# Performance work log

Measured on AMD Instinct MI355X. Metric: run time of the kernel, lower is better.

## Reference

```python
import jax, jax.numpy as jnp
import numpy as np

BATCH, SEQ, D_IN = 4, 2048, 1024
STATE, D_OUT, KX = 1024, 1024, 10


def setup_inputs() -> dict:
    key = jax.random.key(0)
    k0, k1, k2, k3, k4, k5 = jax.random.split(key, 6)
    inputs = jax.random.normal(k0, (BATCH, SEQ, D_IN), jnp.float32)
    h0 = jax.random.normal(k1, (STATE,), jnp.float32)
    A = jax.random.normal(k2, (STATE,), jnp.float32)
    A = A / jnp.max(jnp.abs(A))  # matches init_A / max|init_A|
    B = jax.random.normal(k3, (D_IN, STATE), jnp.float32) / D_IN
    C = jax.random.normal(k4, (STATE, D_OUT), jnp.float32) / STATE
    M = jax.random.normal(k5, (D_IN, D_OUT, KX), jnp.float32) / D_OUT
    return {"inputs": inputs, "h0": h0, "A": A, "B": B, "C": C, "M": M}


def compute_ar_x_preds(w, x):
    # w: (d_out, d_in, k); x: (b, l, d_in)
    d_out, d_in, k = w.shape
    b, l, _ = x.shape
    o = jnp.einsum('oik,bli->bklo', w, x)  # (b, k, l, d_out)
    shifts = jnp.arange(k)
    # roll slice i forward by i along the length axis
    o = jax.vmap(lambda oi, s: jnp.roll(oi, s, axis=1), in_axes=(1, 0), out_axes=1)(o, shifts)
    # triu mask: keep position t in slice i only if t >= i (causal AR)
    m = (jnp.arange(l)[None, :] >= shifts[:, None]).astype(o.dtype)  # (k, l)
    return jnp.sum(o * m[None, :, :, None], axis=1)  # (b, l, d_out)


def reference(inputs, h0, A, B, C, M):
    bsz = inputs.shape[0]
    h_init = jnp.broadcast_to(h0, (bsz, h0.shape[0]))  # h0.expand(bsz, state_dim)
    u_seq = jnp.swapaxes(inputs, 0, 1)  # (l, b, d_in)

    def step(h, u):
        h_new = A * h + u @ B  # diagonal recurrence
        return h_new, h_new

    _, hs = jax.lax.scan(step, h_init, u_seq)  # (l, b, state)
    all_h_t = jnp.swapaxes(hs, 0, 1)  # (b, l, state)
    lds_out = all_h_t @ C  # (b, l, d_out)
    ar = compute_ar_x_preds(M, inputs)
    return lds_out + ar
```

## Files before the change

kernel.cpp:

```cpp
#include <hip/hip_runtime.h>
#include <stdint.h>

typedef unsigned short u16;
typedef __attribute__((ext_vector_type(4))) float f32x4;
typedef __attribute__((ext_vector_type(8))) short s16x8;

#define BATCH 4
#define SEQ   2048
#define DIM   1024
#define KX    10
#define PAD   16
#define SEQP  (SEQ+PAD)

__device__ __forceinline__ u16 f2b(float f) {
    union { float f; uint32_t u; } v; v.f = f;
    uint32_t u = v.u + 0x7fffu + ((v.u >> 16) & 1u);
    return (u16)(u >> 16);
}
__device__ __forceinline__ float b2f(u16 h) {
    union { uint32_t u; float f; } v; v.u = ((uint32_t)h) << 16;
    return v.f;
}

__device__ __forceinline__ void llds16(const u16* g, u16* l) {
    __builtin_amdgcn_global_load_lds(
        (const __attribute__((address_space(1))) uint32_t*)g,
        (__attribute__((address_space(3))) uint32_t*)l, 16, 0, 0);
}

#define PREP_X_END  8256
#define PREP_C_END  10304
#define PREP_M_END  14400

__global__ __launch_bounds__(256) void k_prep(
    const float* __restrict__ x, const float* __restrict__ B,
    const float* __restrict__ C, const float* __restrict__ M,
    u16* __restrict__ Xpad, u16* __restrict__ Btr, u16* __restrict__ Wall)
{
    __shared__ float tile[32][33];
    const int bid = blockIdx.x, tid = threadIdx.x;

    if (bid < PREP_X_END) {
        int idx = bid * 256 + tid;
        long e = (long)idx * 4;
        int i = (int)(e & 1023);
        int row = (int)(e >> 10);
        int t = row % SEQP;
        int b = row / SEQP;
        ushort4 o;
        if (t < PAD) {
            o.x = 0; o.y = 0; o.z = 0; o.w = 0;
        } else {
            const float4 v = *(const float4*)(x + (((long)(b * SEQ + (t - PAD)) << 10) + i));
            o.x = f2b(v.x); o.y = f2b(v.y); o.z = f2b(v.z); o.w = f2b(v.w);
        }
        *(ushort4*)(Xpad + ((long)row << 10) + i) = o;
    } else if (bid < PREP_C_END) {
        const int tb = bid - PREP_X_END;
        const float* in = (tb < 1024) ? B : C;
        u16* out = (tb < 1024) ? Btr : Wall;
        int lb = tb & 1023;
        int bx = lb & 31, by = lb >> 5;
        int tx = tid & 31, ty = tid >> 5;
#pragma unroll
        for (int j = 0; j < 4; j++)
            tile[ty + j * 8][tx] = in[(long)(by * 32 + ty + j * 8) * 1024 + bx * 32 + tx];
        __syncthreads();
#pragma unroll
        for (int j = 0; j < 4; j++)
            out[(long)(bx * 32 + ty + j * 8) * 1024 + by * 32 + tx] = f2b(tile[tx][ty + j * 8]);
    } else {
        int idx = (bid - PREP_C_END) * 256 + tid;
        int o = idx >> 10, i = idx & 1023;
        const float* src = M + (long)idx * KX;
#pragma unroll
        for (int k = 0; k < KX; k++)
            Wall[((long)(k + 1) << 20) + ((long)o << 10) + i] = f2b(src[k]);
    }
}


__global__ void k_scan1(const u16* __restrict__ U, const float* __restrict__ A,
                        float* __restrict__ F) {
    int s = blockIdx.x * 256 + threadIdx.x;
    int bc = blockIdx.y;
    int b = bc >> 4, c = bc & 15;
    float a = A[s];
    const u16* u = U + (((long)(b * SEQ + c * 128)) << 10) + s;
    float f = 0.f;
#pragma unroll 8
    for (int j = 0; j < 128; j++) f = fmaf(a, f, b2f(u[(long)j << 10]));
    F[((long)bc << 10) + s] = f;
}

__global__ void k_scan2(const float* __restrict__ F, const float* __restrict__ A,
                        const float* __restrict__ h0, float* __restrict__ Carry) {
    int idx = blockIdx.x * 256 + threadIdx.x;
    int b = idx >> 10, s = idx & 1023;
    float a = A[s];
    float a128 = a;
#pragma unroll
    for (int q = 0; q < 7; q++) a128 *= a128;
    float carry = h0[s];
#pragma unroll
    for (int c = 0; c < 16; c++) {
        long off = ((long)(b * 16 + c) << 10) + s;
        Carry[off] = carry;
        carry = fmaf(a128, carry, F[off]);
    }
}

__global__ void k_scan3(u16* __restrict__ U, const float* __restrict__ A,
                        const float* __restrict__ Carry) {
    int s = blockIdx.x * 256 + threadIdx.x;
    int bc = blockIdx.y;
    int b = bc >> 4, c = bc & 15;
    float a = A[s];
    long base = (((long)(b * SEQ + c * 128)) << 10) + s;
    float h = Carry[((long)bc << 10) + s];
#pragma unroll 8
    for (int j = 0; j < 128; j++) {
        h = fmaf(a, h, b2f(U[base + ((long)j << 10)]));
        U[base + ((long)j << 10)] = f2b(h);
    }
}

__global__ __launch_bounds__(256, 4) void k_gemm(
    void* __restrict__ outv, const u16* __restrict__ Xpad,
    const u16* __restrict__ Hbf, const u16* __restrict__ W,
    int ngroups, int use_h, int bf16_out)
{
    __shared__ u16 smem[18432];

    const int tid  = threadIdx.x;
    const int wave = tid >> 6, lane = tid & 63;
    const int pair = wave >> 1, wm = wave & 1;
    const int quad = lane >> 4, l15 = lane & 15;

    const int col0 = blockIdx.x * 64;
    const int row0 = blockIdx.y * 128;
    const int bb = row0 >> 11;
    const long Xrow0 = (long)bb * SEQP + PAD + (row0 & (SEQ - 1));
    const long XslabBase = (Xrow0 - 16) << 10;
    const int lastg = ngroups - 1;

    f32x4 acc[4][4];
#pragma unroll
    for (int i = 0; i < 4; i++)
#pragma unroll
        for (int j = 0; j < 4; j++)
            acc[i][j] = (f32x4){0.f, 0.f, 0.f, 0.f};

    auto stageX2 = [&](int k0) {
#pragma unroll
        for (int p = 0; p < 2; p++) {
            const int kb = k0 + p * 512;
            u16* slab = smem + p * 5120;
#pragma unroll
            for (int q = 0; q < 2; q++) {
                int u = q * 256 + tid;
                int row = u >> 2;
                int kc = (u & 3) ^ (row & 3);
                llds16(Xpad + XslabBase + ((long)row << 10) + kb + kc * 8,
                       &slab[(q * 256 + wave * 64) * 8]);
            }
            {
                int u = 512 + tid;
                int row = u >> 2;
                int kc = (u & 3) ^ (row & 3);
                if (tid < 128)
                    llds16(Xpad + XslabBase + ((long)row << 10) + kb + kc * 8,
                           &slab[(512 + wave * 64) * 8]);
            }
        }
    };
    auto stageW2 = [&](int k0, int wsel, int parity) {
        const u16* Wg = W + ((long)wsel << 20) + ((long)col0 << 10);
#pragma unroll
        for (int p = 0; p < 2; p++) {
            int row = tid >> 2;
            int kc = (tid & 3) ^ (row & 3);
            llds16(Wg + ((long)row << 10) + (k0 + p * 512) + kc * 8,
                   &smem[10240 + (p * 2 + parity) * 2048 + wave * 64 * 8]);
        }
    };
    auto stageH2 = [&](int k0) {
        const u16* Hb = Hbf + ((long)row0 << 10);
#pragma unroll
        for (int p = 0; p < 2; p++) {
            const int kb = k0 + p * 512;
            u16* slab = smem + p * 5120;
#pragma unroll
            for (int q = 0; q < 2; q++) {
                int u = q * 256 + tid;
                int row = u >> 2;
                int kc = (u & 3) ^ (row & 3);
                llds16(Hb + ((long)row << 10) + kb + kc * 8,
                       &slab[(q * 256 + wave * 64) * 8]);
            }
        }
    };

    const u16* slab  = smem + pair * 5120;
    const u16* Wpair = smem + 10240 + pair * 2 * 2048;

    for (int k0 = 0; k0 < 512; k0 += 32) {
        stageX2(k0);
        stageW2(k0, use_h ? 1 : 0, 0);
        __syncthreads();

        for (int g = 0; g < ngroups; g++) {
            const bool isH = use_h && (g == lastg);
            if (isH) {
                stageH2(k0);
                __syncthreads();
            }
            if (g < lastg) {
                int gn = g + 1;
                int wsel = use_h ? ((gn == lastg) ? 0 : gn + 1) : gn;
                stageW2(k0, wsel, gn & 1);
            }

            const int rbase = isH ? 0 : (16 - g);
            const u16* Wrd = Wpair + (g & 1) * 2048;

            s16x8 af[4], bfr[4];
#pragma unroll
            for (int mi = 0; mi < 4; mi++) {
                int arow = rbase + wm * 64 + mi * 16 + l15;
                int kca = (quad ^ (arow & 3)) << 3;
                af[mi] = *(const s16x8*)&slab[arow * 32 + kca];
            }
#pragma unroll
            for (int ni = 0; ni < 4; ni++) {
                int brow = ni * 16 + l15;
                int kcb = (quad ^ (brow & 3)) << 3;
                bfr[ni] = *(const s16x8*)&Wrd[brow * 32 + kcb];
            }
#pragma unroll
            for (int mi = 0; mi < 4; mi++)
#pragma unroll
                for (int ni = 0; ni < 4; ni++)
                    acc[mi][ni] = __builtin_amdgcn_mfma_f32_16x16x32_bf16(
                        af[mi], bfr[ni], acc[mi][ni], 0, 0, 0);
            __syncthreads();
        }
    }

    float* scr = (float*)smem;
    if (pair == 1) {
#pragma unroll
        for (int mi = 0; mi < 4; mi++) {
            int rl = wm * 64 + mi * 16 + quad * 4;
#pragma unroll
            for (int ni = 0; ni < 4; ni++) {
                int c = ni * 16 + l15;
                f32x4 v = acc[mi][ni];
#pragma unroll
                for (int reg = 0; reg < 4; reg++)
                    scr[(rl + reg) * 64 + c] = v[reg];
            }
        }
    }
    __syncthreads();
    if (pair == 0) {
#pragma unroll
        for (int mi = 0; mi < 4; mi++) {
            int rl = wm * 64 + mi * 16 + quad * 4;
            int r = row0 + rl;
#pragma unroll
            for (int ni = 0; ni < 4; ni++) {
                int cl = ni * 16 + l15;
                int c = col0 + cl;
                f32x4 v = acc[mi][ni];
                if (bf16_out) {
                    u16* ob = (u16*)outv;
#pragma unroll
                    for (int reg = 0; reg < 4; reg++)
                        ob[((long)(r + reg) << 10) + c] =
                            f2b(v[reg] + scr[(rl + reg) * 64 + cl]);
                } else {
                    float* of = (float*)outv;
#pragma unroll
                    for (int reg = 0; reg < 4; reg++)
                        of[((long)(r + reg) << 10) + c] =
                            v[reg] + scr[(rl + reg) * 64 + cl];
                }
            }
        }
    }
}


extern "C" void kernel_launch(void* const* d_in, const int* in_sizes, int n_in,
                              void* d_out, int out_size, void* d_ws, size_t ws_size,
                              hipStream_t stream) {
    const float* x  = (const float*)d_in[0];
    const float* h0 = (const float*)d_in[1];
    const float* A  = (const float*)d_in[2];
    const float* B  = (const float*)d_in[3];
    const float* C  = (const float*)d_in[4];
    const float* M  = (const float*)d_in[5];
    float* out = (float*)d_out;

    char* ws = (char*)d_ws;
    u16*   Xpad  = (u16*)  (ws);
    u16*   Wall  = (u16*)  (ws + 16908288);
    u16*   Btr   = (u16*)  (ws + 39976960);
    u16*   Ubf   = (u16*)  (ws + 42074112);
    float* F     = (float*)(ws + 58851328);
    float* Carry = (float*)(ws + 59113472);

    k_prep<<<dim3(PREP_M_END), dim3(256), 0, stream>>>(x, B, C, M, Xpad, Btr, Wall);

    k_gemm<<<dim3(16, 64), dim3(256), 0, stream>>>(Ubf, Xpad, Ubf, Btr, 1, 0, 1);

    k_scan1<<<dim3(4, 64), dim3(256), 0, stream>>>(Ubf, A, F);
    k_scan2<<<dim3(16), dim3(256), 0, stream>>>(F, A, h0, Carry);
    k_scan3<<<dim3(4, 64), dim3(256), 0, stream>>>(Ubf, A, Carry);

    k_gemm<<<dim3(16, 64), dim3(256), 0, stream>>>(out, Xpad, Ubf, Wall, 11, 1, 0);
}
```

Measured before the change: 357.1 us.

## Vectorize scan kernels with 8-wide bf16 loads and change LDS swizzle pattern

The chunked scan kernels now process 8 state channels per thread with 16-byte vector loads and stores, using 64-step chunks (32 chunks per batch) instead of 128-step chunks, and scan2 is adjusted to a^64 accordingly. The GEMM's LDS XOR swizzle now uses (row>>1)&3 to cut bank conflicts on the 16-byte fragment reads. F and Carry are moved to reuse the Btr workspace region, which is dead after the first GEMM. The scan kernels launch only 128 blocks of 128 threads, which may underfill the GPU, and the workspace aliasing depends on Btr not being read later.

New measurement: 354.6 us. No clear change (-0.7%).

```diff
diff --git a/kernel.cpp b/kernel.cpp
--- a/kernel.cpp
+++ b/kernel.cpp
@@ -82,15 +82,23 @@
 
 __global__ void k_scan1(const u16* __restrict__ U, const float* __restrict__ A,
                         float* __restrict__ F) {
-    int s = blockIdx.x * 256 + threadIdx.x;
-    int bc = blockIdx.y;
-    int b = bc >> 4, c = bc & 15;
-    float a = A[s];
-    const u16* u = U + (((long)(b * SEQ + c * 128)) << 10) + s;
-    float f = 0.f;
-#pragma unroll 8
-    for (int j = 0; j < 128; j++) f = fmaf(a, f, b2f(u[(long)j << 10]));
-    F[((long)bc << 10) + s] = f;
+    const int sg = threadIdx.x;
+    const int bc = blockIdx.x;
+    const int b = bc >> 5, c = bc & 31;
+    const int s0 = sg << 3;
+    const float4 a0 = *(const float4*)(A + s0);
+    const float4 a1 = *(const float4*)(A + s0 + 4);
+    float a[8] = {a0.x, a0.y, a0.z, a0.w, a1.x, a1.y, a1.z, a1.w};
+    float f[8] = {0.f, 0.f, 0.f, 0.f, 0.f, 0.f, 0.f, 0.f};
+    const u16* u = U + (((long)(b * SEQ + c * 64)) << 10) + s0;
+#pragma unroll 4
+    for (int j = 0; j < 64; j++) {
+        s16x8 v = *(const s16x8*)(u + ((long)j << 10));
+#pragma unroll
+        for (int i = 0; i < 8; i++) f[i] = fmaf(a[i], f[i], b2f((u16)v[i]));
+    }
+    *(float4*)(F + ((long)bc << 10) + s0)     = (float4){f[0], f[1], f[2], f[3]};
+    *(float4*)(F + ((long)bc << 10) + s0 + 4) = (float4){f[4], f[5], f[6], f[7]};
 }
 
 __global__ void k_scan2(const float* __restrict__ F, const float* __restrict__ A,
@@ -98,30 +106,41 @@
     int idx = blockIdx.x * 256 + threadIdx.x;
     int b = idx >> 10, s = idx & 1023;
     float a = A[s];
-    float a128 = a;
-#pragma unroll
-    for (int q = 0; q < 7; q++) a128 *= a128;
+    float a64 = a;
+#pragma unroll
+    for (int q = 0; q < 6; q++) a64 *= a64;
     float carry = h0[s];
 #pragma unroll
-    for (int c = 0; c < 16; c++) {
-        long off = ((long)(b * 16 + c) << 10) + s;
+    for (int c = 0; c < 32; c++) {
+        long off = ((long)(b * 32 + c) << 10) + s;
         Carry[off] = carry;
-        carry = fmaf(a128, carry, F[off]);
+        carry = fmaf(a64, carry, F[off]);
     }
 }
 
 __global__ void k_scan3(u16* __restrict__ U, const float* __restrict__ A,
                         const float* __restrict__ Carry) {
-    int s = blockIdx.x * 256 + threadIdx.x;
-    int bc = blockIdx.y;
-    int b = bc >> 4, c = bc & 15;
-    float a = A[s];
-    long base = (((long)(b * SEQ + c * 128)) << 10) + s;
-    float h = Carry[((long)bc << 10) + s];
-#pragma unroll 8
-    for (int j = 0; j < 128; j++) {
-        h = fmaf(a, h, b2f(U[base + ((long)j << 10)]));
-        U[base + ((long)j << 10)] = f2b(h);
+    const int sg = threadIdx.x;
+    const int bc = blockIdx.x;
+    const int b = bc >> 5, c = bc & 31;
+    const int s0 = sg << 3;
+    const float4 a0 = *(const float4*)(A + s0);
+    const float4 a1 = *(const float4*)(A + s0 + 4);
+    float a[8] = {a0.x, a0.y, a0.z, a0.w, a1.x, a1.y, a1.z, a1.w};
+    float h[8];
+#pragma unroll
+    for (int i = 0; i < 8; i++) h[i] = Carry[((long)bc << 10) + s0 + i];
+    u16* u = U + (((long)(b * SEQ + c * 64)) << 10) + s0;
+#pragma unroll 4
+    for (int j = 0; j < 64; j++) {
+        s16x8 v = *(const s16x8*)(u + ((long)j << 10));
+        s16x8 w;
+#pragma unroll
+        for (int i = 0; i < 8; i++) {
+            h[i] = fmaf(a[i], h[i], b2f((u16)v[i]));
+            w[i] = (short)f2b(h[i]);
+        }
+        *(s16x8*)(u + ((long)j << 10)) = w;
     }
 }
 
@@ -160,14 +179,14 @@
             for (int q = 0; q < 2; q++) {
                 int u = q * 256 + tid;
                 int row = u >> 2;
-                int kc = (u & 3) ^ (row & 3);
+                int kc = (u & 3) ^ ((row >> 1) & 3);
                 llds16(Xpad + XslabBase + ((long)row << 10) + kb + kc * 8,
                        &slab[(q * 256 + wave * 64) * 8]);
             }
             {
                 int u = 512 + tid;
                 int row = u >> 2;
-                int kc = (u & 3) ^ (row & 3);
+                int kc = (u & 3) ^ ((row >> 1) & 3);
                 if (tid < 128)
                     llds16(Xpad + XslabBase + ((long)row << 10) + kb + kc * 8,
                            &slab[(512 + wave * 64) * 8]);
@@ -179,7 +198,7 @@
 #pragma unroll
         for (int p = 0; p < 2; p++) {
             int row = tid >> 2;
-            int kc = (tid & 3) ^ (row & 3);
+            int kc = (tid & 3) ^ ((row >> 1) & 3);
             llds16(Wg + ((long)row << 10) + (k0 + p * 512) + kc * 8,
                    &smem[10240 + (p * 2 + parity) * 2048 + wave * 64 * 8]);
         }
@@ -194,7 +213,7 @@
             for (int q = 0; q < 2; q++) {
                 int u = q * 256 + tid;
                 int row = u >> 2;
-                int kc = (u & 3) ^ (row & 3);
+                int kc = (u & 3) ^ ((row >> 1) & 3);
                 llds16(Hb + ((long)row << 10) + kb + kc * 8,
                        &slab[(q * 256 + wave * 64) * 8]);
             }
@@ -228,13 +247,13 @@
 #pragma unroll
             for (int mi = 0; mi < 4; mi++) {
                 int arow = rbase + wm * 64 + mi * 16 + l15;
-                int kca = (quad ^ (arow & 3)) << 3;
+                int kca = (quad ^ ((arow >> 1) & 3)) << 3;
                 af[mi] = *(const s16x8*)&slab[arow * 32 + kca];
             }
 #pragma unroll
             for (int ni = 0; ni < 4; ni++) {
                 int brow = ni * 16 + l15;
-                int kcb = (quad ^ (brow & 3)) << 3;
+                int kcb = (quad ^ ((brow >> 1) & 3)) << 3;
                 bfr[ni] = *(const s16x8*)&Wrd[brow * 32 + kcb];
             }
 #pragma unroll
@@ -308,16 +327,16 @@
     u16*   Wall  = (u16*)  (ws + 16908288);
     u16*   Btr   = (u16*)  (ws + 39976960);
     u16*   Ubf   = (u16*)  (ws + 42074112);
-    float* F     = (float*)(ws + 58851328);
-    float* Carry = (float*)(ws + 59113472);
+    float* F     = (float*)(ws + 39976960);
+    float* Carry = (float*)(ws + 39976960 + 524288);
 
     k_prep<<<dim3(PREP_M_END), dim3(256), 0, stream>>>(x, B, C, M, Xpad, Btr, Wall);
 
     k_gemm<<<dim3(16, 64), dim3(256), 0, stream>>>(Ubf, Xpad, Ubf, Btr, 1, 0, 1);
 
-    k_scan1<<<dim3(4, 64), dim3(256), 0, stream>>>(Ubf, A, F);
+    k_scan1<<<dim3(128), dim3(128), 0, stream>>>(Ubf, A, F);
     k_scan2<<<dim3(16), dim3(256), 0, stream>>>(F, A, h0, Carry);
-    k_scan3<<<dim3(4, 64), dim3(256), 0, stream>>>(Ubf, A, Carry);
+    k_scan3<<<dim3(128), dim3(128), 0, stream>>>(Ubf, A, Carry);
 
     k_gemm<<<dim3(16, 64), dim3(256), 0, stream>>>(out, Xpad, Ubf, Wall, 11, 1, 0);
 }
```
